# Optimization experiments

Hardware: AMD Instinct MI355X
Metric: run time of the kernel (lower is better)

Reference implementation:

```python
import jax, jax.numpy as jnp
import numpy as np
import math

N, C, W = 4, 768, 2048
H = 12            # num_attention_heads
D = C // H        # attention_head_size = 64
G = 4             # q/k/v groups


def grouped_conv1x1(x, w, b):
    # x: [N, C, W]; w: [G, C/G, C/G] (cout_per_g, cin_per_g); b: [C]
    xg = x.reshape(N, G, C // G, W)
    out = jnp.einsum('goc,ngcw->ngow', w, xg)       # [N, G, C/G, W]
    return out.reshape(N, C, W) + b[None, :, None]


def setup_inputs() -> dict:
    key = jax.random.key(0)
    ks = jax.random.split(key, 7)
    s = 1.0 / math.sqrt(C // G)
    return {
        'hidden_states': jax.random.normal(ks[0], (N, C, W), jnp.float32),
        'attention_mask': jnp.zeros((N, 1, 1, W), jnp.float32),
        'wq': jax.random.normal(ks[1], (G, C // G, C // G), jnp.float32) * s,
        'bq': jax.random.normal(ks[2], (C,), jnp.float32) * 0.02,
        'wk': jax.random.normal(ks[3], (G, C // G, C // G), jnp.float32) * s,
        'bk': jax.random.normal(ks[4], (C,), jnp.float32) * 0.02,
        'wv': jax.random.normal(ks[5], (G, C // G, C // G), jnp.float32) * s,
        'bv': jax.random.normal(ks[6], (C,), jnp.float32) * 0.02,
    }


def reference(hidden_states, attention_mask, wq, bq, wk, bk, wv, bv):
    q = grouped_conv1x1(hidden_states, wq, bq)       # [N, C, W]
    k = grouped_conv1x1(hidden_states, wk, bk)
    v = grouped_conv1x1(hidden_states, wv, bv)
    # transpose_for_scores_conv1d: [N,C,W] -> [N,H,W,D]
    q = q.reshape(N, H, D, W).transpose(0, 1, 3, 2)
    # transpose_key_for_scores_conv1d: [N,C,W] -> [N,H,D,W]
    k = k.reshape(N, H, D, W)
    v = v.reshape(N, H, D, W).transpose(0, 1, 3, 2)
    scores = jnp.einsum('nhqd,nhdk->nhqk', q, k) / math.sqrt(D)
    scores = scores + attention_mask                 # broadcast [N,1,1,W]
    probs = jax.nn.softmax(scores, axis=-1)          # dropout p=0 (eval)
    ctx = jnp.einsum('nhqk,nhkd->nhqd', probs, v)    # [N,H,W,D]
    # transpose_output_conv1d: [N,H,W,D] -> [N,C,W]
    return ctx.transpose(0, 1, 3, 2).reshape(N, C, W)
```

## Files before the change

kernel.cpp:

```cpp
#include <hip/hip_runtime.h>
#include <math.h>

typedef __attribute__((ext_vector_type(4))) float floatx4;
typedef __attribute__((ext_vector_type(8))) short shortx8;
typedef __attribute__((ext_vector_type(4))) short shortx4;

#define NB 4
#define CC 768
#define WW 2048
#define HH 12
#define DD 64
#define GG 4
#define CG 192
#define HPG 3
#define L2E 1.4426950408889634f
#define C18 0.18033688011112043f
#define MSH 11.541560327111707f
#define WSZ (GG * CG * CG)

__device__ __forceinline__ float fast_exp2(float x) {
    return __builtin_amdgcn_exp2f(x);
}

__device__ __forceinline__ short f2bf(float f) {
    union { float f; unsigned u; } v; v.f = f;
    unsigned r = v.u + 0x7fffu + ((v.u >> 16) & 1u);
    return (short)(r >> 16);
}

__device__ __forceinline__ int cvtpk(float lo, float hi) {
    int r;
    asm("v_cvt_pk_bf16_f32 %0, %1, %2" : "=v"(r) : "v"(lo), "v"(hi));
    return r;
}

__device__ __forceinline__ shortx8 mk8(int a, int b, int c, int d) {
    union { int i[4]; shortx8 h; } u;
    u.i[0] = a; u.i[1] = b; u.i[2] = c; u.i[3] = d;
    return u.h;
}

__device__ __forceinline__ int swzK(int r) {
    return (((r & 7) * 2) + ((r >> 3) & 1)) & 7;
}
__device__ __forceinline__ int swzV(int r) {
    return r & 7;
}

__device__ __forceinline__ void gl_lds16(const void* g, void* l) {
    __builtin_amdgcn_global_load_lds(
        (const __attribute__((address_space(1))) unsigned int*)g,
        (__attribute__((address_space(3))) unsigned int*)l, 16, 0, 0);
}

__global__ __launch_bounds__(256) void prep(
    const float* __restrict__ x,
    const float* __restrict__ wq, const float* __restrict__ wk,
    const float* __restrict__ wv,
    short* __restrict__ XTh, short* __restrict__ Wf)
{
    __shared__ short Th[64 * 72];
    const int tid = threadIdx.x;
    const int b   = blockIdx.x;

    if (b < 1536) {
        const int w0 = (b & 31) * 64;
        const int c0 = ((b >> 5) % 12) * 64;
        const int n  = b / 384;
        const int w  = tid & 63;
        const int cb = (tid >> 6) * 16;

        float xv[16];
        #pragma unroll
        for (int j = 0; j < 16; ++j)
            xv[j] = x[((size_t)n * CC + c0 + cb + j) * WW + w0 + w];

        shortx8 hi0, hi1;
        #pragma unroll
        for (int j = 0; j < 8; ++j) { hi0[j] = f2bf(xv[j]); hi1[j] = f2bf(xv[j + 8]); }
        *(shortx8*)&Th[w * 72 + cb]     = hi0;
        *(shortx8*)&Th[w * 72 + cb + 8] = hi1;
        __syncthreads();

        const int wr = tid >> 2;
        const int cc = (tid & 3) * 16;
        const size_t ro = ((size_t)n * WW + w0 + wr) * CC + c0 + cc;
        *(shortx8*)&XTh[ro]     = *(const shortx8*)&Th[wr * 72 + cc];
        *(shortx8*)&XTh[ro + 8] = *(const shortx8*)&Th[wr * 72 + cc + 8];
    } else {
        const int t = (b - 1536) * 256 + tid;
        const int g  = t / (CG * CG);
        const int r  = t - g * (CG * CG);
        const int o  = r / CG;
        const int k  = r - o * CG;
        const int off = (((g * 12 + (o >> 4)) * 6 + (k >> 5)) * 512)
                      + ((k >> 3) & 3) * 128 + (o & 15) * 8 + (k & 7);
        const float* src[3] = {wq, wk, wv};
        #pragma unroll
        for (int m = 0; m < 3; ++m)
            Wf[m * WSZ + off] = f2bf(src[m][t]);
    }
}

__global__ __launch_bounds__(256) void qkv_gemm(
    const short* __restrict__ XTh, const short* __restrict__ Wf,
    const float* __restrict__ bq, const float* __restrict__ bk,
    const float* __restrict__ bv,
    short* __restrict__ Qb, short* __restrict__ Kb, short* __restrict__ Vb)
{
    __shared__ __align__(16) char smem[26112];
    short* Xh_l = (short*)smem;

    const int lin  = blockIdx.x;
    const int xcd  = lin & 7;
    const int iw   = lin >> 3;
    const int mat  = iw % 3;
    const int tile = (iw / 3) * 8 + xcd;
    const int p0   = (tile & 31) * 64;
    const int g    = (tile >> 5) & 3;
    const int n    = tile >> 7;

    const int tid  = threadIdx.x;
    const int wid  = __builtin_amdgcn_readfirstlane(tid >> 6);
    const int lane = tid & 63;
    const int l15  = lane & 15;
    const int quad = lane >> 4;
    const int ob   = wid * 48;

    {
        const short* xhb = XTh + ((size_t)n * WW + p0) * CC + g * CG;
        #pragma unroll
        for (int rd = 0; rd < 6; ++rd) {
            const int Lb = rd * 256 + wid * 64;
            const int L  = Lb + lane;
            const int p  = (L * 2731) >> 16;
            const int sc = L - p * 24;
            const int ss = (sc & ~7) | ((sc & 7) ^ (p & 7));
            gl_lds16(xhb + (size_t)p * CC + ss * 8, &Xh_l[Lb * 8]);
        }
    }
    __syncthreads();

    floatx4 acc[3][4];
    #pragma unroll
    for (int mi = 0; mi < 3; ++mi)
        #pragma unroll
        for (int ni = 0; ni < 4; ++ni) acc[mi][ni] = (floatx4)0.0f;

    const short* wfm = Wf + (size_t)mat * WSZ + lane * 8;

    #pragma unroll
    for (int ks = 0; ks < 6; ++ks) {
        shortx8 ah[3], bh[4];
        #pragma unroll
        for (int mi = 0; mi < 3; ++mi)
            ah[mi] = *(const shortx8*)(wfm + (((g * 12 + wid * 3 + mi) * 6 + ks) << 9));
        #pragma unroll
        for (int ni = 0; ni < 4; ++ni) {
            const int p  = ni * 16 + l15;
            const int vp = (ks >> 1) * 8 + ((((ks & 1) * 4) + quad) ^ (p & 7));
            bh[ni] = *(const shortx8*)&Xh_l[(p * 24 + vp) * 8];
        }
        #pragma unroll
        for (int mi = 0; mi < 3; ++mi)
            #pragma unroll
            for (int ni = 0; ni < 4; ++ni)
                acc[mi][ni] = __builtin_amdgcn_mfma_f32_16x16x32_bf16(ah[mi], bh[ni], acc[mi][ni], 0, 0, 0);
    }

    const float* bias = (mat == 0) ? bq : (mat == 1) ? bk : bv;
    short* Y = (mat == 0) ? Qb : (mat == 1) ? Kb : Vb;

    __syncthreads();

    if (mat < 2) {
        short* T = (short*)smem;
        #pragma unroll
        for (int mi = 0; mi < 3; ++mi) {
            float4 b4 = *(const float4*)&bias[g * CG + ob + mi * 16 + quad * 4];
            const int o = ob + mi * 16 + quad * 4;
            #pragma unroll
            for (int ni = 0; ni < 4; ++ni) {
                const int p = ni * 16 + l15;
                T[p * 200 + o]     = f2bf(acc[mi][ni][0] + b4.x);
                T[p * 200 + o + 1] = f2bf(acc[mi][ni][1] + b4.y);
                T[p * 200 + o + 2] = f2bf(acc[mi][ni][2] + b4.z);
                T[p * 200 + o + 3] = f2bf(acc[mi][ni][3] + b4.w);
            }
        }
        __syncthreads();
        #pragma unroll
        for (int hc = 0; hc < HPG; ++hc) {
            const size_t nh = (size_t)n * HH + g * HPG + hc;
            #pragma unroll
            for (int half = 0; half < 2; ++half) {
                const int idx = tid + half * 256;
                const int p  = idx >> 3;
                const int dc = (idx & 7) * 8;
                *(shortx8*)&Y[(nh * WW + p0 + p) * DD + dc] =
                    *(const shortx8*)&T[p * 200 + hc * 64 + dc];
            }
        }
    } else {
        short* T = (short*)smem;
        #pragma unroll
        for (int mi = 0; mi < 3; ++mi) {
            float4 b4 = *(const float4*)&bias[g * CG + ob + mi * 16 + quad * 4];
            const int o = ob + mi * 16 + quad * 4;
            #pragma unroll
            for (int ni = 0; ni < 4; ++ni) {
                const int p = ni * 16 + l15;
                T[(o)     * 68 + p] = f2bf(acc[mi][ni][0] + b4.x);
                T[(o + 1) * 68 + p] = f2bf(acc[mi][ni][1] + b4.y);
                T[(o + 2) * 68 + p] = f2bf(acc[mi][ni][2] + b4.z);
                T[(o + 3) * 68 + p] = f2bf(acc[mi][ni][3] + b4.w);
            }
        }
        __syncthreads();
        #pragma unroll
        for (int pass = 0; pass < 6; ++pass) {
            const int idx = tid + pass * 256;
            const int o  = idx >> 3;
            const int pc = (idx & 7) * 8;
            const size_t nh = (size_t)n * HH + g * HPG + (o >> 6);
            const int d = o & 63;
            *(shortx8*)&Y[(nh * DD + d) * WW + p0 + pc] =
                *(const shortx8*)&T[o * 68 + pc];
        }
    }
}

#define RST 65

__global__ __launch_bounds__(256) void attn_split(
    const short* __restrict__ Qb, const short* __restrict__ Kb,
    const short* __restrict__ Vb, const float* __restrict__ mask,
    float* __restrict__ out)
{
    __shared__ __align__(16) char smem[40960];
    float* Ml = (float*)(smem + 32768);

    const int lin  = blockIdx.x;
    const int xcd  = lin & 7;
    const int slot = lin >> 3;
    const int pair = xcd * 6 + (slot >> 5);
    const int qt   = slot & 31;
    const int n    = pair / HH;
    const int h    = pair % HH;
    const int q0   = qt * 64;

    const int tid  = threadIdx.x;
    const int wid  = __builtin_amdgcn_readfirstlane(tid >> 6);
    const int lane = tid & 63;
    const int l15  = lane & 15;
    const int quad = lane >> 4;

    const size_t nh = (size_t)n * HH + h;
    const short* Kbase = Kb + nh * WW * DD;
    const short* Vbase = Vb + nh * DD * WW;

    {
        const float* mbase = mask + (size_t)n * WW;
        #pragma unroll
        for (int i = 0; i < WW / 256; ++i)
            Ml[tid + i * 256] = fmaf(mbase[tid + i * 256], L2E, -MSH);
    }

    shortx8 qf[2];
    {
        const short* qp = Qb + (nh * WW + q0 + wid * 16 + l15) * DD + quad * 8;
        qf[0] = *(const shortx8*)(qp);
        qf[1] = *(const shortx8*)(qp + 32);
    }

    shortx8 onef;
    #pragma unroll
    for (int j = 0; j < 8; ++j) onef[j] = (short)0x3F80;

    floatx4 oacc[4];
    #pragma unroll
    for (int nn2 = 0; nn2 < 4; ++nn2) oacc[nn2] = (floatx4)0.0f;
    floatx4 lsum = (floatx4)0.0f;

    const int r0  = wid * 16 + (lane >> 3);
    const int r1  = r0 + 8;
    const int cgk0 = (lane & 7) ^ swzK(r0);
    const int cgk1 = (lane & 7) ^ swzK(r1);
    const int cgv0 = (lane & 7) ^ swzV(r0);
    const int cgv1 = (lane & 7) ^ swzV(r1);
    const short* kp0 = Kbase + (size_t)r0 * DD + cgk0 * 8;
    const short* kp1 = Kbase + (size_t)r1 * DD + cgk1 * 8;
    const short* vp0 = Vbase + (size_t)r0 * WW + cgv0 * 8;
    const short* vp1 = Vbase + (size_t)r1 * WW + cgv1 * 8;
    const int KR0 = (wid * 16) * 64, KR1 = (wid * 16 + 8) * 64;

    const int rowmap = (l15 >> 2) * 8 + (l15 & 3);

    #define STAGE(j, bb)                                                      \
        do {                                                                  \
            short* ksd = (short*)(smem + (bb) * 8192);                        \
            short* vsd = (short*)(smem + 16384 + (bb) * 8192);                \
            gl_lds16(kp0 + (size_t)(j) * 64 * DD, ksd + KR0);                 \
            gl_lds16(kp1 + (size_t)(j) * 64 * DD, ksd + KR1);                 \
            gl_lds16(vp0 + (j) * 64, vsd + KR0);                              \
            gl_lds16(vp1 + (j) * 64, vsd + KR1);                              \
        } while (0)

    STAGE(0, 0);
    __syncthreads();

    for (int kt = 0; kt < WW / 64; ++kt) {
        const int bb = kt & 1;
        if (kt + 1 < WW / 64) STAGE(kt + 1, 1 - bb);

        const short* Ks_l = (const short*)(smem + bb * 8192);
        const short* Vs_l = (const short*)(smem + 16384 + bb * 8192);
        const int k0 = kt * 64;

        shortx8 kf[4][2], vf[4][2];
        #pragma unroll
        for (int jj = 0; jj < 4; ++jj) {
            const int rp = ((jj >> 1) * 32) + ((jj & 1) * 4) + rowmap;
            #pragma unroll
            for (int hf = 0; hf < 2; ++hf)
                kf[jj][hf] = *(const shortx8*)&Ks_l[rp * 64 + (((hf * 4 + quad) ^ swzK(rp)) * 8)];
        }
        #pragma unroll
        for (int nn2 = 0; nn2 < 4; ++nn2) {
            const int r = 16 * nn2 + l15;
            #pragma unroll
            for (int hf = 0; hf < 2; ++hf)
                vf[nn2][hf] = *(const shortx8*)&Vs_l[r * 64 + (((hf * 4 + quad) ^ swzV(r)) * 8)];
        }

        floatx4 mv4[4];
        #pragma unroll
        for (int jj = 0; jj < 4; ++jj) {
            const int kb = ((jj >> 1) * 32) + ((jj & 1) * 4) + quad * 8;
            mv4[jj] = *(const floatx4*)&Ml[k0 + kb];
        }

        floatx4 sacc[4];
        #pragma unroll
        for (int jj = 0; jj < 4; ++jj) {
            sacc[jj] = (floatx4)0.0f;
            sacc[jj] = __builtin_amdgcn_mfma_f32_16x16x32_bf16(kf[jj][0], qf[0], sacc[jj], 0, 0, 0);
            sacc[jj] = __builtin_amdgcn_mfma_f32_16x16x32_bf16(kf[jj][1], qf[1], sacc[jj], 0, 0, 0);
        }

        int s[4][2];
        #pragma unroll
        for (int jj = 0; jj < 4; ++jj) {
            float p0 = fast_exp2(fmaf(sacc[jj][0], C18, mv4[jj][0]));
            float p1 = fast_exp2(fmaf(sacc[jj][1], C18, mv4[jj][1]));
            float p2 = fast_exp2(fmaf(sacc[jj][2], C18, mv4[jj][2]));
            float p3 = fast_exp2(fmaf(sacc[jj][3], C18, mv4[jj][3]));
            s[jj][0] = cvtpk(p0, p1);
            s[jj][1] = cvtpk(p2, p3);
        }
        shortx8 pf0 = mk8(s[0][0], s[0][1], s[1][0], s[1][1]);
        shortx8 pf1 = mk8(s[2][0], s[2][1], s[3][0], s[3][1]);

        #pragma unroll
        for (int nn2 = 0; nn2 < 4; ++nn2) {
            oacc[nn2] = __builtin_amdgcn_mfma_f32_16x16x32_bf16(pf0, vf[nn2][0], oacc[nn2], 0, 0, 0);
            oacc[nn2] = __builtin_amdgcn_mfma_f32_16x16x32_bf16(pf1, vf[nn2][1], oacc[nn2], 0, 0, 0);
        }
        lsum = __builtin_amdgcn_mfma_f32_16x16x32_bf16(pf0, onef, lsum, 0, 0, 0);
        lsum = __builtin_amdgcn_mfma_f32_16x16x32_bf16(pf1, onef, lsum, 0, 0, 0);

        __syncthreads();
    }
    #undef STAGE

    float linv[4];
    #pragma unroll
    for (int r = 0; r < 4; ++r) linv[r] = 1.0f / lsum[r];

    float* Ol = (float*)smem;
    #pragma unroll
    for (int nn2 = 0; nn2 < 4; ++nn2)
        #pragma unroll
        for (int r = 0; r < 4; ++r)
            Ol[(wid * 16 + quad * 4 + r) * RST + nn2 * 16 + l15] = oacc[nn2][r] * linv[r];
    __syncthreads();

    float* obase = out + (nh * DD) * WW + q0;
    #pragma unroll
    for (int it = 0; it < 4; ++it) {
        const int idx = tid + it * 256;
        const int q4 = (idx & 15) * 4;
        const int d  = idx >> 4;
        floatx4 v;
        #pragma unroll
        for (int i = 0; i < 4; ++i) v[i] = Ol[(q4 + i) * RST + d];
        *(floatx4*)&obase[(size_t)d * WW + q4] = v;
    }
}

extern "C" void kernel_launch(void* const* d_in, const int* in_sizes, int n_in,
                              void* d_out, int out_size, void* d_ws, size_t ws_size,
                              hipStream_t stream) {
    const float* x    = (const float*)d_in[0];
    const float* mask = (const float*)d_in[1];
    const float* wq   = (const float*)d_in[2];
    const float* bq   = (const float*)d_in[3];
    const float* wk   = (const float*)d_in[4];
    const float* bk   = (const float*)d_in[5];
    const float* wv   = (const float*)d_in[6];
    const float* bv   = (const float*)d_in[7];
    float* out = (float*)d_out;

    const size_t per = (size_t)NB * HH * WW * DD;
    short* Qb  = (short*)d_ws;
    short* Kb  = Qb + per;
    short* Vb  = Kb + per;
    short* XTh = Vb + per;
    short* Wfp = XTh + per;

    hipLaunchKernelGGL(prep, dim3(1536 + WSZ / 256), dim3(256), 0, stream,
                       x, wq, wk, wv, XTh, Wfp);
    hipLaunchKernelGGL(qkv_gemm, dim3(1536), dim3(256), 0, stream,
                       XTh, Wfp, bq, bk, bv, Qb, Kb, Vb);
    hipLaunchKernelGGL(attn_split, dim3(1536), dim3(256), 0, stream,
                       Qb, Kb, Vb, mask, out);
}
```

Before: 180.9 us.

## Fuse input transpose and bf16 conversion into QKV GEMM tile load

```diff
diff --git a/kernel.cpp b/kernel.cpp
--- a/kernel.cpp
+++ b/kernel.cpp
@@ -53,63 +53,32 @@
         (__attribute__((address_space(3))) unsigned int*)l, 16, 0, 0);
 }
 
-__global__ __launch_bounds__(256) void prep(
-    const float* __restrict__ x,
+__global__ __launch_bounds__(256) void prep_w(
     const float* __restrict__ wq, const float* __restrict__ wk,
-    const float* __restrict__ wv,
-    short* __restrict__ XTh, short* __restrict__ Wf)
+    const float* __restrict__ wv, short* __restrict__ Wf)
 {
-    __shared__ short Th[64 * 72];
-    const int tid = threadIdx.x;
-    const int b   = blockIdx.x;
-
-    if (b < 1536) {
-        const int w0 = (b & 31) * 64;
-        const int c0 = ((b >> 5) % 12) * 64;
-        const int n  = b / 384;
-        const int w  = tid & 63;
-        const int cb = (tid >> 6) * 16;
-
-        float xv[16];
-        #pragma unroll
-        for (int j = 0; j < 16; ++j)
-            xv[j] = x[((size_t)n * CC + c0 + cb + j) * WW + w0 + w];
-
-        shortx8 hi0, hi1;
-        #pragma unroll
-        for (int j = 0; j < 8; ++j) { hi0[j] = f2bf(xv[j]); hi1[j] = f2bf(xv[j + 8]); }
-        *(shortx8*)&Th[w * 72 + cb]     = hi0;
-        *(shortx8*)&Th[w * 72 + cb + 8] = hi1;
-        __syncthreads();
-
-        const int wr = tid >> 2;
-        const int cc = (tid & 3) * 16;
-        const size_t ro = ((size_t)n * WW + w0 + wr) * CC + c0 + cc;
-        *(shortx8*)&XTh[ro]     = *(const shortx8*)&Th[wr * 72 + cc];
-        *(shortx8*)&XTh[ro + 8] = *(const shortx8*)&Th[wr * 72 + cc + 8];
-    } else {
-        const int t = (b - 1536) * 256 + tid;
-        const int g  = t / (CG * CG);
-        const int r  = t - g * (CG * CG);
-        const int o  = r / CG;
-        const int k  = r - o * CG;
-        const int off = (((g * 12 + (o >> 4)) * 6 + (k >> 5)) * 512)
-                      + ((k >> 3) & 3) * 128 + (o & 15) * 8 + (k & 7);
-        const float* src[3] = {wq, wk, wv};
-        #pragma unroll
-        for (int m = 0; m < 3; ++m)
-            Wf[m * WSZ + off] = f2bf(src[m][t]);
-    }
+    const int t = blockIdx.x * 256 + threadIdx.x;
+    const int g  = t / (CG * CG);
+    const int r  = t - g * (CG * CG);
+    const int o  = r / CG;
+    const int k  = r - o * CG;
+    const int off = (((g * 12 + (o >> 4)) * 6 + (k >> 5)) * 512)
+                  + ((k >> 3) & 3) * 128 + (o & 15) * 8 + (k & 7);
+    const float* src[3] = {wq, wk, wv};
+    #pragma unroll
+    for (int m = 0; m < 3; ++m)
+        Wf[m * WSZ + off] = f2bf(src[m][t]);
 }
 
 __global__ __launch_bounds__(256) void qkv_gemm(
-    const short* __restrict__ XTh, const short* __restrict__ Wf,
+    const float* __restrict__ x, const short* __restrict__ Wf,
     const float* __restrict__ bq, const float* __restrict__ bk,
     const float* __restrict__ bv,
     short* __restrict__ Qb, short* __restrict__ Kb, short* __restrict__ Vb)
 {
-    __shared__ __align__(16) char smem[26112];
+    __shared__ __align__(16) char smem[33792];
     short* Xh_l = (short*)smem;
+    short* Th   = (short*)(smem + 24576);
 
     const int lin  = blockIdx.x;
     const int xcd  = lin & 7;
@@ -128,18 +97,32 @@
     const int ob   = wid * 48;
 
     {
-        const short* xhb = XTh + ((size_t)n * WW + p0) * CC + g * CG;
-        #pragma unroll
-        for (int rd = 0; rd < 6; ++rd) {
-            const int Lb = rd * 256 + wid * 64;
-            const int L  = Lb + lane;
-            const int p  = (L * 2731) >> 16;
-            const int sc = L - p * 24;
-            const int ss = (sc & ~7) | ((sc & 7) ^ (p & 7));
-            gl_lds16(xhb + (size_t)p * CC + ss * 8, &Xh_l[Lb * 8]);
-        }
-    }
-    __syncthreads();
+        const int w  = tid & 63;
+        const int cb = (tid >> 6) * 16;
+        const int wr = tid >> 2;
+        const int cc = (tid & 3) * 16;
+        for (int s = 0; s < 3; ++s) {
+            const float* xb = x + ((size_t)n * CC + g * CG + s * 64 + cb) * WW + p0 + w;
+            float xv[16];
+            #pragma unroll
+            for (int j = 0; j < 16; ++j) xv[j] = xb[(size_t)j * WW];
+            shortx8 h0, h1;
+            #pragma unroll
+            for (int j = 0; j < 8; ++j) { h0[j] = f2bf(xv[j]); h1[j] = f2bf(xv[j + 8]); }
+            *(shortx8*)&Th[w * 72 + cb]     = h0;
+            *(shortx8*)&Th[w * 72 + cb + 8] = h1;
+            __syncthreads();
+            shortx8 v0 = *(const shortx8*)&Th[wr * 72 + cc];
+            shortx8 v1 = *(const shortx8*)&Th[wr * 72 + cc + 8];
+            const int ch0 = s * 8 + (cc >> 3);
+            const int ch1 = ch0 + 1;
+            const int sc0 = (ch0 & ~7) | ((ch0 & 7) ^ (wr & 7));
+            const int sc1 = (ch1 & ~7) | ((ch1 & 7) ^ (wr & 7));
+            *(shortx8*)&Xh_l[(wr * 24 + sc0) * 8] = v0;
+            *(shortx8*)&Xh_l[(wr * 24 + sc1) * 8] = v1;
+            __syncthreads();
+        }
+    }
 
     floatx4 acc[3][4];
     #pragma unroll
@@ -415,13 +398,12 @@
     short* Qb  = (short*)d_ws;
     short* Kb  = Qb + per;
     short* Vb  = Kb + per;
-    short* XTh = Vb + per;
-    short* Wfp = XTh + per;
-
-    hipLaunchKernelGGL(prep, dim3(1536 + WSZ / 256), dim3(256), 0, stream,
-                       x, wq, wk, wv, XTh, Wfp);
+    short* Wfp = Vb + per;
+
+    hipLaunchKernelGGL(prep_w, dim3(WSZ / 256), dim3(256), 0, stream,
+                       wq, wk, wv, Wfp);
     hipLaunchKernelGGL(qkv_gemm, dim3(1536), dim3(256), 0, stream,
-                       XTh, Wfp, bq, bk, bv, Qb, Kb, Vb);
+                       x, Wfp, bq, bk, bv, Qb, Kb, Vb);
     hipLaunchKernelGGL(attn_split, dim3(1536), dim3(256), 0, stream,
                        Qb, Kb, Vb, mask, out);
 }
```

Measured after the change: 178.2 us. About the same (-1.5%).
